# Kernel tuning notes

Measured on AMD Instinct MI355X. Metric: run time of the kernel, lower is better.

The kernel has to match this reference:

```python
import jax, jax.numpy as jnp
import numpy as np

D_MODEL = 1024
NUM_HEADS = 16
NUM_GROUPS = 4
HEAD_DIM = D_MODEL // NUM_HEADS
ROPE_BASE = 10000.0


def _rope_tables(seq_len, head_dim, dtype=jnp.float32):
    inv_freq = 1.0 / (ROPE_BASE ** (jnp.arange(0, head_dim, 2, dtype=jnp.float32) / head_dim))
    freqs = jnp.arange(seq_len, dtype=jnp.float32)[:, None] * inv_freq[None, :]  # [S, hd/2]
    emb = jnp.concatenate([freqs, freqs], axis=-1)  # [S, hd]
    return jnp.cos(emb).astype(dtype), jnp.sin(emb).astype(dtype)


def _rotate_half(t):
    half = t.shape[-1] // 2
    return jnp.concatenate([-t[..., half:], t[..., :half]], axis=-1)


def _apply_rope(t, cos, sin):
    # t: [B,S,H,hd]; cos/sin: [S,hd] broadcast over batch and heads
    c = cos[None, :, None, :]
    s = sin[None, :, None, :]
    return t * c + _rotate_half(t) * s


def setup_inputs() -> dict:
    key = jax.random.key(0)
    ks = jax.random.split(key, 5)
    B, S, D = 2, 2048, D_MODEL
    scale = 1.0 / np.sqrt(D)
    return {
        "x": jax.random.normal(ks[0], (B, S, D), dtype=jnp.float32),
        "Wq": jax.random.normal(ks[1], (D, D), dtype=jnp.float32) * scale,
        "Wk": jax.random.normal(ks[2], (D, D), dtype=jnp.float32) * scale,
        "Wv": jax.random.normal(ks[3], (D, D), dtype=jnp.float32) * scale,
        "Wo": jax.random.normal(ks[4], (D, D), dtype=jnp.float32) * scale,
    }


def reference(x, Wq, Wk, Wv, Wo):
    B, S, D = x.shape
    H, G, hd = NUM_HEADS, NUM_GROUPS, HEAD_DIM
    hpg = H // G  # heads per group

    q = (x @ Wq.T).reshape(B, S, H, hd)
    k = (x @ Wk.T).reshape(B, S, H, hd)
    v = (x @ Wv.T).reshape(B, S, H, hd)

    cos, sin = _rope_tables(S, hd, x.dtype)
    q = _apply_rope(q, cos, sin)
    k = _apply_rope(k, cos, sin)

    # query head reordering: [B,S,G,hpg,hd] -> transpose(2,3) -> [B,S,H,hd]
    q = q.reshape(B, S, G, hpg, hd).swapaxes(2, 3).reshape(B, S, H, hd)
    # GQA group-mean of K/V, then repeat back to H heads
    k = k.reshape(B, S, G, hpg, hd).mean(axis=3)  # [B,S,G,hd]
    v = v.reshape(B, S, G, hpg, hd).mean(axis=3)
    k = jnp.repeat(k, hpg, axis=2)  # [B,S,H,hd]
    v = jnp.repeat(v, hpg, axis=2)

    q = q.transpose(0, 2, 1, 3)  # [B,H,S,hd]
    k = k.transpose(0, 2, 1, 3)
    v = v.transpose(0, 2, 1, 3)

    scores = jnp.einsum('bhqd,bhkd->bhqk', q, k) / np.sqrt(hd)  # [B,H,S,S]
    probs = jax.nn.softmax(scores, axis=-1)
    attn = jnp.einsum('bhqk,bhkd->bhqd', probs, v)

    attn = attn.transpose(0, 2, 1, 3).reshape(B, S, D)
    return attn @ Wo.T
```

## Files before the change

### kernel.cpp

```cpp
#include <hip/hip_runtime.h>
#include <hip/hip_bf16.h>
#include <math.h>

#define B_ 2
#define S_ 2048
#define D_ 1024
#define H_ 16
#define G_ 4
#define HD_ 64

typedef float f32x4  __attribute__((ext_vector_type(4)));
typedef float f32x16 __attribute__((ext_vector_type(16)));
typedef short s16x8  __attribute__((ext_vector_type(8)));
typedef unsigned short u16x4 __attribute__((ext_vector_type(4)));
typedef unsigned int   u32x4 __attribute__((ext_vector_type(4)));

__device__ __forceinline__ unsigned short f2b(float f) {
    __hip_bfloat16 h = __float2bfloat16(f);
    return __builtin_bit_cast(unsigned short, h);
}
__device__ __forceinline__ unsigned cvtpk(float lo, float hi) {
    unsigned r;
    asm("v_cvt_pk_bf16_f32 %0, %1, %2" : "=v"(r) : "v"(lo), "v"(hi));
    return r;
}
__device__ __forceinline__ void plswap(unsigned &a, unsigned &b) {
    asm("v_permlane32_swap_b32 %0, %1" : "+v"(a), "+v"(b));
}

#define MFMA16(a, b, c) __builtin_amdgcn_mfma_f32_16x16x32_bf16(a, b, c, 0, 0, 0)
#define MFMA32(a, b, c) __builtin_amdgcn_mfma_f32_32x32x16_bf16(a, b, c, 0, 0, 0)

#define GLOAD16(gp, lp) __builtin_amdgcn_global_load_lds(                      \
    (const __attribute__((address_space(1))) void*)(gp),                      \
    (__attribute__((address_space(3))) void*)(lp), 16, 0, 0)

__global__ __launch_bounds__(256)
void prep_all(const float* __restrict__ x,  const float* __restrict__ Wq,
              const float* __restrict__ Wk, const float* __restrict__ Wv,
              const float* __restrict__ Wo,
              unsigned short* __restrict__ xb, unsigned short* __restrict__ wb,
              unsigned short* __restrict__ wob,
              float* __restrict__ cost, float* __restrict__ sint)
{
    const int NQ_WB = (1536*1024)/4;
    const int NQ_WO = (1024*1024)/4;
    const int NQ_X  = (B_*S_*D_)/4;
    int q = blockIdx.x*256 + threadIdx.x;
    if (q < NQ_WB) {
        const int idx = q*4, row = idx >> 10, c = idx & 1023;
        u16x4 o;
        if (row < 1024) {
            f32x4 v = *(const f32x4*)&Wq[(size_t)row*1024 + c];
            #pragma unroll
            for (int j = 0; j < 4; ++j) o[j] = f2b(v[j]);
        } else {
            const int rd = row - 1024, kv = rd >> 8, gd = rd & 255;
            const int g = gd >> 6, d = gd & 63;
            const float* W = kv ? Wv : Wk;
            f32x4 sum = {0.f, 0.f, 0.f, 0.f};
            #pragma unroll
            for (int p = 0; p < 4; ++p)
                sum += *(const f32x4*)&W[(size_t)((g*4 + p)*64 + d)*1024 + c];
            #pragma unroll
            for (int j = 0; j < 4; ++j) o[j] = f2b(sum[j]*0.25f);
        }
        *(u16x4*)&wb[idx] = o;
        return;
    }
    q -= NQ_WB;
    if (q < NQ_WO) {
        const int idx = q*4;
        f32x4 v = *(const f32x4*)&Wo[idx];
        u16x4 o;
        #pragma unroll
        for (int j = 0; j < 4; ++j) o[j] = f2b(v[j]);
        *(u16x4*)&wob[idx] = o;
        return;
    }
    q -= NQ_WO;
    if (q < NQ_X) {
        const int idx = q*4;
        f32x4 v = *(const f32x4*)&x[idx];
        u16x4 o;
        #pragma unroll
        for (int j = 0; j < 4; ++j) o[j] = f2b(v[j]);
        *(u16x4*)&xb[idx] = o;
        return;
    }
    q -= NQ_X;
    if (q < (S_*32)/4) {
        const int idx = q*4, s = idx >> 5, f0 = idx & 31;
        #pragma unroll
        for (int j = 0; j < 4; ++j) {
            const float f = (float)(f0 + j);
            const float fr = (float)s * powf(10000.0f, -f*(1.0f/32.0f));
            cost[idx + j] = cosf(fr);
            sint[idx + j] = sinf(fr);
        }
    }
}

template<int MODE>
__global__ __launch_bounds__(256)
void gemm_mfma(const unsigned short* __restrict__ Am,
               const unsigned short* __restrict__ Bm,
               unsigned short* __restrict__ qr,
               unsigned short* __restrict__ kr,
               unsigned short* __restrict__ vt,
               float* __restrict__ outf,
               const float* __restrict__ cost,
               const float* __restrict__ sint,
               int nbx)
{
    __shared__ unsigned short As[2][128*64];
    __shared__ unsigned short Bs[2][128*64];

    const int nwg = gridDim.x;
    const int cpx = nwg >> 3;
    const int bid = blockIdx.x;
    const int swz = (bid & 7)*cpx + (bid >> 3);
    const int bx = swz % nbx, by = swz / nbx;

    const int t  = threadIdx.x;
    const int w  = t >> 6, l = t & 63;
    const int lg = l >> 4, lr = l & 15;
    const int wr = w >> 1, wc = w & 1;

    const unsigned short* gA = Am + (size_t)by*128*D_;
    const unsigned short* gB = Bm + (size_t)bx*128*D_;

    const int srow = l >> 3;
    const int schk = (l & 7) ^ srow;

#define STAGE(buf, k0)                                                         \
    _Pragma("unroll")                                                          \
    for (int i_ = 0; i_ < 4; ++i_) {                                           \
        const int row_ = 32*w + 8*i_ + srow;                                   \
        GLOAD16(gA + (size_t)row_*D_ + (k0) + 8*schk, &As[buf][(32*w + 8*i_)*64]); \
        GLOAD16(gB + (size_t)row_*D_ + (k0) + 8*schk, &Bs[buf][(32*w + 8*i_)*64]); \
    }

    f32x4 acc[4][4] = {};

    STAGE(0, 0);
    #pragma unroll 1
    for (int kt = 0; kt < 16; ++kt) {
        const int cur = kt & 1;
        if (kt < 15) {
            STAGE(cur ^ 1, 64*(kt + 1));
            asm volatile("s_waitcnt vmcnt(8)" ::: "memory");
        } else {
            asm volatile("s_waitcnt vmcnt(0)" ::: "memory");
        }
        __builtin_amdgcn_s_barrier();

        #pragma unroll
        for (int kk = 0; kk < 2; ++kk) {
            s16x8 af[4], bfr[4];
            #pragma unroll
            for (int m = 0; m < 4; ++m) {
                const int row = 64*wr + 16*m + lr;
                af[m] = *(const s16x8*)&As[cur][row*64 + 8*((lg + 4*kk) ^ (row & 7))];
            }
            #pragma unroll
            for (int n = 0; n < 4; ++n) {
                const int col = 64*wc + 16*n + lr;
                bfr[n] = *(const s16x8*)&Bs[cur][col*64 + 8*((lg + 4*kk) ^ (col & 7))];
            }
            #pragma unroll
            for (int m = 0; m < 4; ++m)
                #pragma unroll
                for (int n = 0; n < 4; ++n)
                    acc[m][n] = MFMA16(af[m], bfr[n], acc[m][n]);
        }
        asm volatile("s_waitcnt lgkmcnt(0)" ::: "memory");
        __builtin_amdgcn_s_barrier();
    }
#undef STAGE

    if (MODE == 1) {
        #pragma unroll
        for (int m = 0; m < 4; ++m)
            #pragma unroll
            for (int r = 0; r < 4; ++r) {
                const int row = by*128 + 64*wr + 16*m + 4*lg + r;
                #pragma unroll
                for (int n = 0; n < 4; ++n)
                    outf[(size_t)row*D_ + bx*128 + 64*wc + 16*n + lr] = acc[m][n][r];
            }
        return;
    }

    if (bx < 10) {
        #pragma unroll
        for (int m = 0; m < 4; ++m) {
            #pragma unroll
            for (int r = 0; r < 4; ++r) {
                const int row = by*128 + 64*wr + 16*m + 4*lg + r;
                const int b = row >> 11, s = row & (S_ - 1);
                const float c_lo = cost[s*32 + lr],      s_lo = sint[s*32 + lr];
                const float c_hi = cost[s*32 + 16 + lr], s_hi = sint[s*32 + 16 + lr];
                unsigned short vals[4];
                #pragma unroll
                for (int n = 0; n < 4; ++n) {
                    const float cc = (n & 1) ? c_hi : c_lo;
                    const float sn = (n & 1) ? s_hi : s_lo;
                    const float self = acc[m][n][r], part = acc[m][n ^ 2][r];
                    const float rv = (n < 2) ? fmaf(self, cc, -part*sn)
                                             : fmaf(self, cc,  part*sn);
                    vals[n] = f2b(rv);
                }
                size_t base;
                unsigned short* dst;
                if (bx < 8) {
                    const int hh = 2*bx + wc;
                    const int hp = (hh & 3)*4 + (hh >> 2);
                    base = (((size_t)b*H_ + hp)*S_ + s)*HD_;
                    dst = qr;
                } else {
                    const int g = (bx - 8)*2 + wc;
                    base = (((size_t)b*G_ + g)*S_ + s)*HD_;
                    dst = kr;
                }
                #pragma unroll
                for (int n = 0; n < 4; ++n) dst[base + 16*n + lr] = vals[n];
            }
        }
    } else {
        const int g = (bx - 10)*2 + wc;
        #pragma unroll
        for (int m = 0; m < 4; ++m) {
            const int row0 = by*128 + 64*wr + 16*m + 4*lg;
            const int b = row0 >> 11, s0 = row0 & (S_ - 1);
            #pragma unroll
            for (int n = 0; n < 4; ++n) {
                const int dd = 16*n + lr;
                u16x4 v;
                #pragma unroll
                for (int r = 0; r < 4; ++r) v[r] = f2b(acc[m][n][r]);
                *(u16x4*)&vt[(((size_t)b*G_ + g)*HD_ + dd)*S_ + s0] = v;
            }
        }
    }
}

__device__ __forceinline__ void stage_tile(const unsigned short* Kp, const unsigned short* Vp,
                                           unsigned short* ksbuf, unsigned short* vsbuf,
                                           int kt, int w, int l)
{
    const int srow = l >> 3;
    const int schk = (l & 7) ^ srow;
    #pragma unroll
    for (int i = 0; i < 2; ++i) {
        const int row = 16*w + 8*i + srow;
        const unsigned short* gk = Kp + ((size_t)(kt*64 + row))*HD_ + 8*schk;
        const unsigned short* gv = Vp + (size_t)row*S_ + kt*64 + 8*schk;
        GLOAD16(gk, ksbuf + (16*w + 8*i)*64);
        GLOAD16(gv, vsbuf + (16*w + 8*i)*64);
    }
}

__global__ __launch_bounds__(256)
void flash_attn_mfma(const unsigned short* __restrict__ qr,
                     const unsigned short* __restrict__ kr,
                     const unsigned short* __restrict__ vt,
                     unsigned short* __restrict__ attnb)
{
    __shared__ unsigned short Ks[2][64*64];
    __shared__ unsigned short Vs[2][64*64];
    __shared__ float xbuf[4][32];

    const int nqt = S_/128;
    const int bid = blockIdx.x;
    const int cpx = gridDim.x >> 3;
    const int swz = (bid & 7)*cpx + (bid >> 3);
    const int qt = swz % nqt;
    const int h  = (swz/nqt) % H_;
    const int b  = swz/(nqt*H_);
    const int g  = h >> 2;
    const int t  = threadIdx.x;
    const int w  = t >> 6;
    const int l  = t & 63;
    const int hi = l >> 5;
    const int li = l & 31;

    const unsigned short* Qp = qr + (((size_t)b*H_ + h)*S_ + (size_t)qt*128 + w*32)*HD_;
    const unsigned short* Kp = kr + ((size_t)b*G_ + g)*(size_t)S_*HD_;
    const unsigned short* Vp = vt + ((size_t)b*G_ + g)*(size_t)HD_*S_;

    s16x8 qf[4];
    #pragma unroll
    for (int kk = 0; kk < 4; ++kk)
        qf[kk] = *(const s16x8*)(Qp + (size_t)li*HD_ + 16*kk + 8*hi);

    f32x16 o[2];
    #pragma unroll
    for (int dt = 0; dt < 2; ++dt)
        #pragma unroll
        for (int e = 0; e < 16; ++e) o[dt][e] = 0.f;
    float m = 0.f, ld = 0.f;

    const float C   = 0.18033688011112044f;
    const float THR = 32.0f;
    const int   NT  = S_/64;

    stage_tile(Kp, Vp, Ks[0], Vs[0], 0, w, l);

    #pragma unroll 1
    for (int kt = 0; kt < NT; ++kt) {
        const int cur = kt & 1;
        if (kt + 1 < NT) {
            stage_tile(Kp, Vp, Ks[cur^1], Vs[cur^1], kt + 1, w, l);
            asm volatile("s_waitcnt vmcnt(4)" ::: "memory");
        } else {
            asm volatile("s_waitcnt vmcnt(0)" ::: "memory");
        }
        __builtin_amdgcn_s_barrier();

        #pragma unroll
        for (int kt2 = 0; kt2 < 2; ++kt2) {
            f32x16 sc;
            #pragma unroll
            for (int e = 0; e < 16; ++e) sc[e] = 0.f;
            #pragma unroll
            for (int kk = 0; kk < 4; ++kk) {
                const int row = 32*kt2 + li;
                s16x8 kf = *(const s16x8*)&Ks[cur][row*64 + 8*((hi + 2*kk) ^ (li & 7))];
                sc = MFMA32(kf, qf[kk], sc);
            }

            float pmax = sc[0];
            #pragma unroll
            for (int r = 1; r < 16; ++r) pmax = fmaxf(pmax, sc[r]);
            pmax = fmaxf(pmax, __shfl_xor(pmax, 32, 64));

            if (__any((pmax > m + THR) ? 1 : 0)) {
                const float mn = fmaxf(m, pmax);
                const float al = __builtin_amdgcn_exp2f((m - mn)*C);
                m = mn; ld *= al;
                xbuf[w][li] = al;
                #pragma unroll
                for (int j = 0; j < 4; ++j) {
                    f32x4 av = *(const f32x4*)&xbuf[w][8*j + 4*hi];
                    #pragma unroll
                    for (int rr = 0; rr < 4; ++rr) {
                        o[0][4*j + rr] *= av[rr];
                        o[1][4*j + rr] *= av[rr];
                    }
                }
            }

            const float nmC = -m*C;
            float p[16];
            float rsum = 0.f;
            #pragma unroll
            for (int r = 0; r < 16; ++r) {
                p[r] = __builtin_amdgcn_exp2f(fmaf(sc[r], C, nmC));
                rsum += p[r];
            }
            ld += rsum + __shfl_xor(rsum, 32, 64);

            #pragma unroll
            for (int s2 = 0; s2 < 2; ++s2) {
                unsigned wa = cvtpk(p[8*s2 + 0], p[8*s2 + 1]);
                unsigned wb = cvtpk(p[8*s2 + 2], p[8*s2 + 3]);
                unsigned wc2 = cvtpk(p[8*s2 + 4], p[8*s2 + 5]);
                unsigned wd = cvtpk(p[8*s2 + 6], p[8*s2 + 7]);
                plswap(wa, wc2);
                plswap(wb, wd);
                u32x4 paw = {wa, wb, wc2, wd};
                s16x8 pa = __builtin_bit_cast(s16x8, paw);

                const int ks = 2*kt2 + s2;
                #pragma unroll
                for (int dt = 0; dt < 2; ++dt) {
                    const int row = li + 32*dt;
                    s16x8 vf = *(const s16x8*)&Vs[cur][row*64 + 8*((hi + 2*ks) ^ (li & 7))];
                    o[dt] = MFMA32(pa, vf, o[dt]);
                }
            }
        }
        asm volatile("s_waitcnt lgkmcnt(0)" ::: "memory");
        __builtin_amdgcn_s_barrier();
    }

    xbuf[w][li] = ld;
    #pragma unroll
    for (int j = 0; j < 4; ++j) {
        f32x4 lv = *(const f32x4*)&xbuf[w][8*j + 4*hi];
        #pragma unroll
        for (int rr = 0; rr < 4; ++rr) {
            const int r  = 4*j + rr;
            const int qq = 8*j + 4*hi + rr;
            const int s  = qt*128 + w*32 + qq;
            const float inv = 1.0f / lv[rr];
            #pragma unroll
            for (int dt = 0; dt < 2; ++dt)
                attnb[((size_t)b*S_ + s)*D_ + h*HD_ + li + 32*dt] = f2b(o[dt][r]*inv);
        }
    }
}

extern "C" void kernel_launch(void* const* d_in, const int* in_sizes, int n_in,
                              void* d_out, int out_size, void* d_ws, size_t ws_size,
                              hipStream_t stream)
{
    const float* x  = (const float*)d_in[0];
    const float* Wq = (const float*)d_in[1];
    const float* Wk = (const float*)d_in[2];
    const float* Wv = (const float*)d_in[3];
    const float* Wo = (const float*)d_in[4];
    float* out = (float*)d_out;

    char* p = (char*)d_ws;
    unsigned short* xb    = (unsigned short*)p; p += (size_t)B_*S_*D_*2;
    unsigned short* wb    = (unsigned short*)p; p += (size_t)1536*1024*2;
    unsigned short* wob   = (unsigned short*)p; p += (size_t)1024*1024*2;
    unsigned short* qr    = (unsigned short*)p; p += (size_t)B_*H_*S_*HD_*2;
    unsigned short* kr    = (unsigned short*)p; p += (size_t)B_*G_*S_*HD_*2;
    unsigned short* vt    = (unsigned short*)p; p += (size_t)B_*G_*HD_*S_*2;
    unsigned short* attnb = (unsigned short*)p; p += (size_t)B_*S_*D_*2;
    float* cost = (float*)p; p += (size_t)S_*32*4;
    float* sint = (float*)p;

    prep_all<<<6720, 256, 0, stream>>>(x, Wq, Wk, Wv, Wo, xb, wb, wob, cost, sint);
    gemm_mfma<0><<<32*12, 256, 0, stream>>>(xb, wb, qr, kr, vt, nullptr, cost, sint, 12);
    flash_attn_mfma<<<B_*H_*(S_/128), 256, 0, stream>>>(qr, kr, vt, attnb);
    gemm_mfma<1><<<32*8, 256, 0, stream>>>(attnb, wob, nullptr, nullptr, nullptr, out, cost, sint, 8);
}
```

Baseline: 112.1 us.

## Enlarge flash-attention KV tile to 128 keys and batch two score tiles per reduction

Doubles the K/V LDS tile to 128 keys per barrier iteration, with a new swizzled V staging layout. It computes two 32-key score MFMA chains together and does one max/sum reduction per 64 keys, using permlane32 swaps instead of cross-lane shuffles. It also adds s_setprio around MFMA sections. This is meant to cut barrier and reduction overhead and raise instruction-level parallelism, at the cost of doubled LDS use (64KB) and more registers, which may reduce occupancy.

```diff
diff --git a/kernel.cpp b/kernel.cpp
--- a/kernel.cpp
+++ b/kernel.cpp
@@ -26,6 +26,13 @@
 }
 __device__ __forceinline__ void plswap(unsigned &a, unsigned &b) {
     asm("v_permlane32_swap_b32 %0, %1" : "+v"(a), "+v"(b));
+}
+__device__ __forceinline__ void plswapf(float &a, float &b) {
+    unsigned ua = __builtin_bit_cast(unsigned, a);
+    unsigned ub = __builtin_bit_cast(unsigned, b);
+    plswap(ua, ub);
+    a = __builtin_bit_cast(float, ua);
+    b = __builtin_bit_cast(float, ub);
 }
 
 #define MFMA16(a, b, c) __builtin_amdgcn_mfma_f32_16x16x32_bf16(a, b, c, 0, 0, 0)
@@ -245,19 +252,20 @@
     }
 }
 
-__device__ __forceinline__ void stage_tile(const unsigned short* Kp, const unsigned short* Vp,
-                                           unsigned short* ksbuf, unsigned short* vsbuf,
-                                           int kt, int w, int l)
+__device__ __forceinline__ void stage128(const unsigned short* Kp, const unsigned short* Vp,
+                                         unsigned short* ks, unsigned short* vs,
+                                         int kt, int w, int l)
 {
     const int srow = l >> 3;
     const int schk = (l & 7) ^ srow;
+    const int vrow = l >> 4;
     #pragma unroll
-    for (int i = 0; i < 2; ++i) {
-        const int row = 16*w + 8*i + srow;
-        const unsigned short* gk = Kp + ((size_t)(kt*64 + row))*HD_ + 8*schk;
-        const unsigned short* gv = Vp + (size_t)row*S_ + kt*64 + 8*schk;
-        GLOAD16(gk, ksbuf + (16*w + 8*i)*64);
-        GLOAD16(gv, vsbuf + (16*w + 8*i)*64);
+    for (int i = 0; i < 4; ++i) {
+        const int krow = 32*w + 8*i + srow;
+        GLOAD16(Kp + ((size_t)(kt*128 + krow))*HD_ + 8*schk, ks + (32*w + 8*i)*64);
+        const int d    = 16*w + 4*i + vrow;
+        const int vchk = (l & 15) ^ (d & 7);
+        GLOAD16(Vp + (size_t)d*S_ + kt*128 + 8*vchk, vs + (16*w + 4*i)*128);
     }
 }
 
@@ -267,8 +275,8 @@
                      const unsigned short* __restrict__ vt,
                      unsigned short* __restrict__ attnb)
 {
-    __shared__ unsigned short Ks[2][64*64];
-    __shared__ unsigned short Vs[2][64*64];
+    __shared__ unsigned short Ks[2][128*64];
+    __shared__ unsigned short Vs[2][64*128];
     __shared__ float xbuf[4][32];
 
     const int nqt = S_/128;
@@ -303,38 +311,49 @@
 
     const float C   = 0.18033688011112044f;
     const float THR = 32.0f;
-    const int   NT  = S_/64;
-
-    stage_tile(Kp, Vp, Ks[0], Vs[0], 0, w, l);
+    const int   NT  = S_/128;
+
+    stage128(Kp, Vp, Ks[0], Vs[0], 0, w, l);
 
     #pragma unroll 1
     for (int kt = 0; kt < NT; ++kt) {
         const int cur = kt & 1;
         if (kt + 1 < NT) {
-            stage_tile(Kp, Vp, Ks[cur^1], Vs[cur^1], kt + 1, w, l);
-            asm volatile("s_waitcnt vmcnt(4)" ::: "memory");
+            stage128(Kp, Vp, Ks[cur^1], Vs[cur^1], kt + 1, w, l);
+            asm volatile("s_waitcnt vmcnt(8)" ::: "memory");
         } else {
             asm volatile("s_waitcnt vmcnt(0)" ::: "memory");
         }
         __builtin_amdgcn_s_barrier();
 
         #pragma unroll
-        for (int kt2 = 0; kt2 < 2; ++kt2) {
-            f32x16 sc;
-            #pragma unroll
-            for (int e = 0; e < 16; ++e) sc[e] = 0.f;
+        for (int half = 0; half < 2; ++half) {
+            f32x16 sc0, sc1;
+            #pragma unroll
+            for (int e = 0; e < 16; ++e) { sc0[e] = 0.f; sc1[e] = 0.f; }
+            __builtin_amdgcn_s_setprio(1);
             #pragma unroll
             for (int kk = 0; kk < 4; ++kk) {
-                const int row = 32*kt2 + li;
-                s16x8 kf = *(const s16x8*)&Ks[cur][row*64 + 8*((hi + 2*kk) ^ (li & 7))];
-                sc = MFMA32(kf, qf[kk], sc);
-            }
-
-            float pmax = sc[0];
-            #pragma unroll
-            for (int r = 1; r < 16; ++r) pmax = fmaxf(pmax, sc[r]);
-            pmax = fmaxf(pmax, __shfl_xor(pmax, 32, 64));
-
+                const int chk = 8*((hi + 2*kk) ^ (li & 7));
+                s16x8 kf0 = *(const s16x8*)&Ks[cur][(64*half      + li)*64 + chk];
+                s16x8 kf1 = *(const s16x8*)&Ks[cur][(64*half + 32 + li)*64 + chk];
+                sc0 = MFMA32(kf0, qf[kk], sc0);
+                sc1 = MFMA32(kf1, qf[kk], sc1);
+            }
+            __builtin_amdgcn_s_setprio(0);
+
+            float mx[8];
+            #pragma unroll
+            for (int i = 0; i < 8; ++i)
+                mx[i] = fmaxf(fmaxf(sc0[i], sc0[i+8]), fmaxf(sc1[i], sc1[i+8]));
+            #pragma unroll
+            for (int i = 0; i < 4; ++i) mx[i] = fmaxf(mx[i], mx[i+4]);
+            float pmax = fmaxf(fmaxf(mx[0], mx[1]), fmaxf(mx[2], mx[3]));
+            {
+                float pa_ = pmax, pb_ = pmax;
+                plswapf(pa_, pb_);
+                pmax = fmaxf(pa_, pb_);
+            }
             if (__any((pmax > m + THR) ? 1 : 0)) {
                 const float mn = fmaxf(m, pmax);
                 const float al = __builtin_amdgcn_exp2f((m - mn)*C);
@@ -352,34 +371,58 @@
             }
 
             const float nmC = -m*C;
-            float p[16];
-            float rsum = 0.f;
+            float p0[16], p1[16];
             #pragma unroll
             for (int r = 0; r < 16; ++r) {
-                p[r] = __builtin_amdgcn_exp2f(fmaf(sc[r], C, nmC));
-                rsum += p[r];
-            }
-            ld += rsum + __shfl_xor(rsum, 32, 64);
-
+                p0[r] = __builtin_amdgcn_exp2f(fmaf(sc0[r], C, nmC));
+                p1[r] = __builtin_amdgcn_exp2f(fmaf(sc1[r], C, nmC));
+            }
+            float s8[8];
+            #pragma unroll
+            for (int i = 0; i < 8; ++i)
+                s8[i] = (p0[i] + p0[i+8]) + (p1[i] + p1[i+8]);
+            #pragma unroll
+            for (int i = 0; i < 4; ++i) s8[i] += s8[i+4];
+            float rsum = (s8[0] + s8[1]) + (s8[2] + s8[3]);
+            {
+                float ca = rsum, cb = rsum;
+                plswapf(ca, cb);
+                ld += ca + cb;
+            }
+
+            __builtin_amdgcn_s_setprio(1);
             #pragma unroll
             for (int s2 = 0; s2 < 2; ++s2) {
-                unsigned wa = cvtpk(p[8*s2 + 0], p[8*s2 + 1]);
-                unsigned wb = cvtpk(p[8*s2 + 2], p[8*s2 + 3]);
-                unsigned wc2 = cvtpk(p[8*s2 + 4], p[8*s2 + 5]);
-                unsigned wd = cvtpk(p[8*s2 + 6], p[8*s2 + 7]);
-                plswap(wa, wc2);
-                plswap(wb, wd);
-                u32x4 paw = {wa, wb, wc2, wd};
-                s16x8 pa = __builtin_bit_cast(s16x8, paw);
-
-                const int ks = 2*kt2 + s2;
+                unsigned a0 = cvtpk(p0[8*s2+0], p0[8*s2+1]);
+                unsigned a1 = cvtpk(p0[8*s2+2], p0[8*s2+3]);
+                unsigned a2 = cvtpk(p0[8*s2+4], p0[8*s2+5]);
+                unsigned a3 = cvtpk(p0[8*s2+6], p0[8*s2+7]);
+                plswap(a0, a2); plswap(a1, a3);
+                u32x4 aw = {a0, a1, a2, a3};
+                s16x8 paf = __builtin_bit_cast(s16x8, aw);
+                const int ksA = 4*half + s2;
                 #pragma unroll
                 for (int dt = 0; dt < 2; ++dt) {
-                    const int row = li + 32*dt;
-                    s16x8 vf = *(const s16x8*)&Vs[cur][row*64 + 8*((hi + 2*ks) ^ (li & 7))];
-                    o[dt] = MFMA32(pa, vf, o[dt]);
+                    const int d = li + 32*dt;
+                    s16x8 vf = *(const s16x8*)&Vs[cur][d*128 + 8*((hi + 2*ksA) ^ (li & 7))];
+                    o[dt] = MFMA32(paf, vf, o[dt]);
                 }
-            }
+                unsigned b0 = cvtpk(p1[8*s2+0], p1[8*s2+1]);
+                unsigned b1 = cvtpk(p1[8*s2+2], p1[8*s2+3]);
+                unsigned b2 = cvtpk(p1[8*s2+4], p1[8*s2+5]);
+                unsigned b3 = cvtpk(p1[8*s2+6], p1[8*s2+7]);
+                plswap(b0, b2); plswap(b1, b3);
+                u32x4 bw = {b0, b1, b2, b3};
+                s16x8 pbf = __builtin_bit_cast(s16x8, bw);
+                const int ksB = 4*half + 2 + s2;
+                #pragma unroll
+                for (int dt = 0; dt < 2; ++dt) {
+                    const int d = li + 32*dt;
+                    s16x8 vf = *(const s16x8*)&Vs[cur][d*128 + 8*((hi + 2*ksB) ^ (li & 7))];
+                    o[dt] = MFMA32(pbf, vf, o[dt]);
+                }
+            }
+            __builtin_amdgcn_s_setprio(0);
         }
         asm volatile("s_waitcnt lgkmcnt(0)" ::: "memory");
         __builtin_amdgcn_s_barrier();
```

Result: faster. 108.5 us (median of 5 runs) (-3.2%).
